# Performance work log

Measured on AMD Instinct MI355X. Metric: run time of the kernel, lower is better.

The kernel has to match this reference:

```python
import jax, jax.numpy as jnp
import numpy as np

N_EDGES = 1_600_000
N_NODES = 100_000
N_GRAPH = 8
D_EDGE = 16
D_NODE = 16
D_GLOB = 16
D_IN = D_EDGE + 2 * D_NODE + D_GLOB  # 64, concat width
D_HID = 64
D_OUT = 16


def setup_inputs() -> dict:
    key = jax.random.key(0)
    ks = jax.random.split(key, 12)
    edges = jax.random.normal(ks[0], (N_EDGES, D_EDGE), dtype=jnp.float32)
    nodes = jax.random.normal(ks[1], (N_NODES, D_NODE), dtype=jnp.float32)
    globals_ = jax.random.normal(ks[2], (N_GRAPH, D_GLOB), dtype=jnp.float32)
    senders = jax.random.randint(ks[3], (N_EDGES,), 0, N_NODES, dtype=jnp.int32)
    receivers = jax.random.randint(ks[4], (N_EDGES,), 0, N_NODES, dtype=jnp.int32)
    edge_graph_ids = jnp.sort(jax.random.randint(ks[5], (N_EDGES,), 0, N_GRAPH, dtype=jnp.int32))
    s0 = 1.0 / np.sqrt(D_IN)
    s1 = 1.0 / np.sqrt(D_HID)
    W0 = jax.random.uniform(ks[6], (D_IN, D_HID), jnp.float32, -s0, s0)
    b0 = jax.random.uniform(ks[7], (D_HID,), jnp.float32, -s0, s0)
    W1 = jax.random.uniform(ks[8], (D_HID, D_HID), jnp.float32, -s1, s1)
    b1 = jax.random.uniform(ks[9], (D_HID,), jnp.float32, -s1, s1)
    W2 = jax.random.uniform(ks[10], (D_HID, D_OUT), jnp.float32, -s1, s1)
    b2 = jax.random.uniform(ks[11], (D_OUT,), jnp.float32, -s1, s1)
    return {"edges": edges, "nodes": nodes, "globals_": globals_,
            "W0": W0, "b0": b0, "W1": W1, "b1": b1, "W2": W2, "b2": b2,
            "senders": senders, "receivers": receivers,
            "edge_graph_ids": edge_graph_ids}


def reference(edges, nodes, globals_, W0, b0, W1, b1, W2, b2,
              senders, receivers, edge_graph_ids):
    # broadcast_receiver/sender_nodes_to_edges: gather node feats per edge
    recv = jnp.take(nodes, receivers, axis=0)          # [E, D_NODE]
    send = jnp.take(nodes, senders, axis=0)            # [E, D_NODE]
    # broadcast_globals_to_edges: repeat(globals, n_edge) == gather by graph id
    glob = jnp.take(globals_, edge_graph_ids, axis=0)  # [E, D_GLOB]
    x = jnp.concatenate([edges, recv, send, glob], axis=-1)  # [E, 64]
    # edge MLP: two hidden relu blocks then output linear (norm='none')
    h = jax.nn.relu(x @ W0 + b0)
    h = jax.nn.relu(h @ W1 + b1)
    return h @ W2 + b2  # updated edges [E, D_OUT]
```

## Files before the change

### kernel.cpp

```cpp
#include <hip/hip_runtime.h>
#include <hip/hip_bf16.h>


typedef float f32x4 __attribute__((ext_vector_type(4)));
typedef short short8 __attribute__((ext_vector_type(8)));

__device__ __forceinline__ unsigned short f2bf(float f) {
    union { float f; unsigned int u; } v; v.f = f;
    unsigned int u = v.u;
    u += 0x7FFFu + ((u >> 16) & 1u);
    return (unsigned short)(u >> 16);
}
__device__ __forceinline__ float bf2f(unsigned short b) {
    union { unsigned int u; float f; } v; v.u = ((unsigned int)b) << 16;
    return v.f;
}
__device__ __forceinline__ void bfsplit(float v, unsigned short& h, unsigned short& l) {
    union { __hip_bfloat16 b; unsigned short u; } ch, cl;
    ch.b = __float2bfloat16(v);
    float r = v - __bfloat162float(ch.b);
    cl.b = __float2bfloat16(r);
    h = ch.u; l = cl.u;
}

__global__ void prep_kernel(const float* __restrict__ W0, const float* __restrict__ b0,
                            const float* __restrict__ W1, const float* __restrict__ b1,
                            const float* __restrict__ W2, const float* __restrict__ b2,
                            void* __restrict__ ws) {
    unsigned short* w0h = (unsigned short*)ws;
    unsigned short* w0l = w0h + 4096;
    unsigned short* w1h = w0h + 8192;
    unsigned short* w1l = w0h + 12288;
    unsigned short* w2h = w0h + 16384;
    unsigned short* w2l = w0h + 17408;
    float* b0f = (float*)(w0h + 18432);
    float* b1f = b0f + 1024;
    float* b2f = b0f + 2048;
    const int tid = blockIdx.x * blockDim.x + threadIdx.x;
    const int gstride = gridDim.x * blockDim.x;

    for (int idx = tid; idx < 4096; idx += gstride) {
        int j = idx & 7, lane = (idx >> 3) & 63, f = idx >> 9;
        int t = f >> 1, kt = f & 1, mr = lane & 15, g = lane >> 4;
        float w = W0[(32 * kt + 8 * g + j) * 64 + (16 * t + mr)];
        unsigned short h = f2bf(w);
        w0h[idx] = h;
        w0l[idx] = f2bf(w - bf2f(h));
    }
    for (int idx = tid; idx < 4096; idx += gstride) {
        int j = idx & 7, lane = (idx >> 3) & 63, f = idx >> 9;
        int t = f >> 1, kt = f & 1, mr = lane & 15, g = lane >> 4;
        int mu = 16 * (2 * kt + (j >> 2)) + 4 * g + (j & 3);
        float w = W1[mu * 64 + (16 * t + mr)];
        unsigned short h = f2bf(w);
        w1h[idx] = h;
        w1l[idx] = f2bf(w - bf2f(h));
    }
    for (int idx = tid; idx < 1024; idx += gstride) {
        int j = idx & 7, lane = (idx >> 3) & 63, kt = idx >> 9;
        int mr = lane & 15, g = lane >> 4;
        int mu = 16 * (2 * kt + (j >> 2)) + 4 * g + (j & 3);
        float w = W2[mu * 16 + mr];
        unsigned short h = f2bf(w);
        w2h[idx] = h;
        w2l[idx] = f2bf(w - bf2f(h));
    }
    for (int idx = tid; idx < 1024; idx += gstride) {
        int lane = idx >> 4, tr = idx & 15;
        int g = lane >> 4, t = tr >> 2, r = tr & 3;
        b0f[idx] = b0[16 * t + 4 * g + r];
        b1f[idx] = b1[16 * t + 4 * g + r];
    }
    for (int idx = tid; idx < 256; idx += gstride) {
        int lane = idx >> 2, r = idx & 3, g = lane >> 4;
        b2f[idx] = b2[4 * g + r];
    }
}

__global__ __launch_bounds__(256, 2) void edge_mlp_kernel(
    const float* __restrict__ edges, const float* __restrict__ nodes,
    const float* __restrict__ globals_, const int* __restrict__ senders,
    const int* __restrict__ receivers, const int* __restrict__ gids,
    const void* __restrict__ ws, float* __restrict__ out, int n_tiles, int iters) {

    const unsigned short* w0h = (const unsigned short*)ws;
    const unsigned short* w0l = w0h + 4096;
    const unsigned short* w1h = w0h + 8192;
    const unsigned short* w1l = w0h + 12288;
    const unsigned short* w2h = w0h + 16384;
    const unsigned short* w2l = w0h + 17408;
    const float* b0f = (const float*)(w0h + 18432);
    const float* b1f = b0f + 1024;
    const float* b2f = b0f + 2048;

    const int lane = threadIdx.x & 63;
    const int wv = threadIdx.x >> 6;
    const int mr = lane & 15;
    const int g = lane >> 4;

    short8 W0H[4][2], W0L[4][2], W1H[4][2], W1L[4][2], W2H[2], W2L[2];
#pragma unroll
    for (int t = 0; t < 4; ++t)
#pragma unroll
        for (int kt = 0; kt < 2; ++kt) {
            int o = ((t * 2 + kt) * 64 + lane) * 8;
            W0H[t][kt] = *(const short8*)(w0h + o);
            W0L[t][kt] = *(const short8*)(w0l + o);
            W1H[t][kt] = *(const short8*)(w1h + o);
            W1L[t][kt] = *(const short8*)(w1l + o);
        }
#pragma unroll
    for (int kt = 0; kt < 2; ++kt) {
        int o = (kt * 64 + lane) * 8;
        W2H[kt] = *(const short8*)(w2h + o);
        W2L[kt] = *(const short8*)(w2l + o);
    }
    float B0[16], B1[16], B2[4];
#pragma unroll
    for (int i = 0; i < 16; ++i) { B0[i] = b0f[lane * 16 + i]; B1[i] = b1f[lane * 16 + i]; }
#pragma unroll
    for (int i = 0; i < 4; ++i) B2[i] = b2f[lane * 4 + i];

    const int W = gridDim.x << 2;
    const int wave_id = (blockIdx.x << 2) | wv;
    const int last = n_tiles - 1;

    #define TILE_OF(i) (((wave_id + (i) * W) < n_tiles) ? (wave_id + (i) * W) : last)

    int e_cur = TILE_OF(0) * 16 + mr;
    {
        int ri = receivers[e_cur], si = senders[e_cur], gi = gids[e_cur];
        (void)ri; (void)si; (void)gi;
    }
    int ri0 = receivers[e_cur], si0 = senders[e_cur], gi0 = gids[e_cur];
    const float* p0 = (g < 2) ? (edges + (size_t)e_cur * 16 + 8 * g)
                              : (nodes + (size_t)ri0 * 16 + 8 * (g - 2));
    const float* p1 = (g < 2) ? (nodes + (size_t)si0 * 16 + 8 * g)
                              : (globals_ + (size_t)gi0 * 16 + 8 * (g - 2));
    f32x4 x0 = *(const f32x4*)p0;
    f32x4 x1 = *(const f32x4*)(p0 + 4);
    f32x4 x2 = *(const f32x4*)p1;
    f32x4 x3 = *(const f32x4*)(p1 + 4);

    int e_nxt = TILE_OF(1) * 16 + mr;
    int ri_n = receivers[e_nxt], si_n = senders[e_nxt], gi_n = gids[e_nxt];

    for (int i = 0; i < iters; ++i) {
        const float* q0 = (g < 2) ? (edges + (size_t)e_nxt * 16 + 8 * g)
                                  : (nodes + (size_t)ri_n * 16 + 8 * (g - 2));
        const float* q1 = (g < 2) ? (nodes + (size_t)si_n * 16 + 8 * g)
                                  : (globals_ + (size_t)gi_n * 16 + 8 * (g - 2));
        f32x4 n0 = *(const f32x4*)q0;
        f32x4 n1 = *(const f32x4*)(q0 + 4);
        f32x4 n2 = *(const f32x4*)q1;
        f32x4 n3 = *(const f32x4*)(q1 + 4);

        int e_nn = TILE_OF(i + 2) * 16 + mr;
        int ri_nn = receivers[e_nn], si_nn = senders[e_nn], gi_nn = gids[e_nn];

        float xs[16];
#pragma unroll
        for (int k = 0; k < 4; ++k) { xs[k] = x0[k]; xs[4 + k] = x1[k]; xs[8 + k] = x2[k]; xs[12 + k] = x3[k]; }
        short8 XH[2], XL[2];
#pragma unroll
        for (int kt = 0; kt < 2; ++kt)
#pragma unroll
            for (int j = 0; j < 8; ++j) {
                unsigned short h, l;
                bfsplit(xs[kt * 8 + j], h, l);
                XH[kt][j] = (short)h;
                XL[kt][j] = (short)l;
            }

        short8 HH[2], HL[2];
#pragma unroll
        for (int t = 0; t < 4; ++t) {
            f32x4 a = {B0[t * 4 + 0], B0[t * 4 + 1], B0[t * 4 + 2], B0[t * 4 + 3]};
            a = __builtin_amdgcn_mfma_f32_16x16x32_bf16(W0L[t][0], XH[0], a, 0, 0, 0);
            a = __builtin_amdgcn_mfma_f32_16x16x32_bf16(W0L[t][1], XH[1], a, 0, 0, 0);
            a = __builtin_amdgcn_mfma_f32_16x16x32_bf16(W0H[t][0], XL[0], a, 0, 0, 0);
            a = __builtin_amdgcn_mfma_f32_16x16x32_bf16(W0H[t][1], XL[1], a, 0, 0, 0);
            a = __builtin_amdgcn_mfma_f32_16x16x32_bf16(W0H[t][0], XH[0], a, 0, 0, 0);
            a = __builtin_amdgcn_mfma_f32_16x16x32_bf16(W0H[t][1], XH[1], a, 0, 0, 0);
#pragma unroll
            for (int r = 0; r < 4; ++r) {
                float v = fmaxf(a[r], 0.0f);
                int kt = t >> 1, j = ((t & 1) << 2) | r;
                unsigned short h, l;
                bfsplit(v, h, l);
                HH[kt][j] = (short)h;
                HL[kt][j] = (short)l;
            }
        }

        short8 GH[2], GL[2];
#pragma unroll
        for (int t = 0; t < 4; ++t) {
            f32x4 a = {B1[t * 4 + 0], B1[t * 4 + 1], B1[t * 4 + 2], B1[t * 4 + 3]};
            a = __builtin_amdgcn_mfma_f32_16x16x32_bf16(W1L[t][0], HH[0], a, 0, 0, 0);
            a = __builtin_amdgcn_mfma_f32_16x16x32_bf16(W1L[t][1], HH[1], a, 0, 0, 0);
            a = __builtin_amdgcn_mfma_f32_16x16x32_bf16(W1H[t][0], HL[0], a, 0, 0, 0);
            a = __builtin_amdgcn_mfma_f32_16x16x32_bf16(W1H[t][1], HL[1], a, 0, 0, 0);
            a = __builtin_amdgcn_mfma_f32_16x16x32_bf16(W1H[t][0], HH[0], a, 0, 0, 0);
            a = __builtin_amdgcn_mfma_f32_16x16x32_bf16(W1H[t][1], HH[1], a, 0, 0, 0);
#pragma unroll
            for (int r = 0; r < 4; ++r) {
                float v = fmaxf(a[r], 0.0f);
                int kt = t >> 1, j = ((t & 1) << 2) | r;
                unsigned short h, l;
                bfsplit(v, h, l);
                GH[kt][j] = (short)h;
                GL[kt][j] = (short)l;
            }
        }

        f32x4 o = {B2[0], B2[1], B2[2], B2[3]};
        o = __builtin_amdgcn_mfma_f32_16x16x32_bf16(W2L[0], GH[0], o, 0, 0, 0);
        o = __builtin_amdgcn_mfma_f32_16x16x32_bf16(W2L[1], GH[1], o, 0, 0, 0);
        o = __builtin_amdgcn_mfma_f32_16x16x32_bf16(W2H[0], GL[0], o, 0, 0, 0);
        o = __builtin_amdgcn_mfma_f32_16x16x32_bf16(W2H[1], GL[1], o, 0, 0, 0);
        o = __builtin_amdgcn_mfma_f32_16x16x32_bf16(W2H[0], GH[0], o, 0, 0, 0);
        o = __builtin_amdgcn_mfma_f32_16x16x32_bf16(W2H[1], GH[1], o, 0, 0, 0);

        __builtin_nontemporal_store(o, (f32x4*)(out + (size_t)e_cur * 16 + 4 * g));

        e_cur = e_nxt;
        x0 = n0; x1 = n1; x2 = n2; x3 = n3;
        e_nxt = e_nn; ri_n = ri_nn; si_n = si_nn; gi_n = gi_nn;
    }
    #undef TILE_OF
}

extern "C" void kernel_launch(void* const* d_in, const int* in_sizes, int n_in,
                              void* d_out, int out_size, void* d_ws, size_t ws_size,
                              hipStream_t stream) {
    const float* edges    = (const float*)d_in[0];
    const float* nodes    = (const float*)d_in[1];
    const float* globals_ = (const float*)d_in[2];
    const float* W0 = (const float*)d_in[3];
    const float* b0 = (const float*)d_in[4];
    const float* W1 = (const float*)d_in[5];
    const float* b1 = (const float*)d_in[6];
    const float* W2 = (const float*)d_in[7];
    const float* b2 = (const float*)d_in[8];
    const int* senders   = (const int*)d_in[9];
    const int* receivers = (const int*)d_in[10];
    const int* gids      = (const int*)d_in[11];
    float* out = (float*)d_out;

    const int n_edges = in_sizes[9];
    const int n_tiles = n_edges >> 4;

    prep_kernel<<<72, 256, 0, stream>>>(W0, b0, W1, b1, W2, b2, d_ws);

    int grid = 2500;
    if (grid > (n_tiles + 3) / 4) grid = (n_tiles + 3) / 4;
    const int waves = grid * 4;
    const int iters = (n_tiles + waves - 1) / waves;
    edge_mlp_kernel<<<grid, 256, 0, stream>>>(edges, nodes, globals_, senders, receivers,
                                              gids, d_ws, out, n_tiles, iters);
}
```

Measured before the change: 282.2 us.

## Stage split-bf16 weights in LDS, pack conversions, dual accumulators, raise occupancy

New measurement: 518.1 us. 83.6% more time.

```diff
diff --git a/kernel.cpp b/kernel.cpp
--- a/kernel.cpp
+++ b/kernel.cpp
@@ -4,23 +4,34 @@
 
 typedef float f32x4 __attribute__((ext_vector_type(4)));
 typedef short short8 __attribute__((ext_vector_type(8)));
+typedef unsigned int u32;
+typedef unsigned int u32x4 __attribute__((ext_vector_type(4)));
 
 __device__ __forceinline__ unsigned short f2bf(float f) {
-    union { float f; unsigned int u; } v; v.f = f;
-    unsigned int u = v.u;
+    union { float f; u32 u; } v; v.f = f;
+    u32 u = v.u;
     u += 0x7FFFu + ((u >> 16) & 1u);
     return (unsigned short)(u >> 16);
 }
 __device__ __forceinline__ float bf2f(unsigned short b) {
-    union { unsigned int u; float f; } v; v.u = ((unsigned int)b) << 16;
+    union { u32 u; float f; } v; v.u = ((u32)b) << 16;
     return v.f;
 }
-__device__ __forceinline__ void bfsplit(float v, unsigned short& h, unsigned short& l) {
-    union { __hip_bfloat16 b; unsigned short u; } ch, cl;
-    ch.b = __float2bfloat16(v);
-    float r = v - __bfloat162float(ch.b);
-    cl.b = __float2bfloat16(r);
-    h = ch.u; l = cl.u;
+__device__ __forceinline__ u32 pk2(float a, float b) {
+    union { __hip_bfloat162 v; u32 u; } c;
+    c.v = __float22bfloat162_rn(make_float2(a, b));
+    return c.u;
+}
+__device__ __forceinline__ float lo_f(u32 p) { union { u32 u; float f; } c; c.u = p << 16; return c.f; }
+__device__ __forceinline__ float hi_f(u32 p) { union { u32 u; float f; } c; c.u = p & 0xffff0000u; return c.f; }
+__device__ __forceinline__ void split4(f32x4 v, u32& h0, u32& h1, u32& l0, u32& l1) {
+    h0 = pk2(v[0], v[1]);
+    h1 = pk2(v[2], v[3]);
+    l0 = pk2(v[0] - lo_f(h0), v[1] - hi_f(h0));
+    l1 = pk2(v[2] - lo_f(h1), v[3] - hi_f(h1));
+}
+__device__ __forceinline__ short8 s8(u32 a, u32 b, u32 c, u32 d) {
+    union { u32x4 u; short8 s; } t; t.u = u32x4{a, b, c, d}; return t.s;
 }
 
 __global__ void prep_kernel(const float* __restrict__ W0, const float* __restrict__ b0,
@@ -66,8 +77,8 @@
         w2l[idx] = f2bf(w - bf2f(h));
     }
     for (int idx = tid; idx < 1024; idx += gstride) {
-        int lane = idx >> 4, tr = idx & 15;
-        int g = lane >> 4, t = tr >> 2, r = tr & 3;
+        int t = idx >> 8, lane = (idx >> 2) & 63, r = idx & 3;
+        int g = lane >> 4;
         b0f[idx] = b0[16 * t + 4 * g + r];
         b1f[idx] = b1[16 * t + 4 * g + r];
     }
@@ -77,61 +88,40 @@
     }
 }
 
-__global__ __launch_bounds__(256, 2) void edge_mlp_kernel(
+__global__ __launch_bounds__(256, 3) void edge_mlp_kernel(
     const float* __restrict__ edges, const float* __restrict__ nodes,
     const float* __restrict__ globals_, const int* __restrict__ senders,
     const int* __restrict__ receivers, const int* __restrict__ gids,
     const void* __restrict__ ws, float* __restrict__ out, int n_tiles, int iters) {
 
-    const unsigned short* w0h = (const unsigned short*)ws;
-    const unsigned short* w0l = w0h + 4096;
-    const unsigned short* w1h = w0h + 8192;
-    const unsigned short* w1l = w0h + 12288;
-    const unsigned short* w2h = w0h + 16384;
-    const unsigned short* w2l = w0h + 17408;
-    const float* b0f = (const float*)(w0h + 18432);
-    const float* b1f = b0f + 1024;
-    const float* b2f = b0f + 2048;
+    __shared__ f32x4 smem4[2880];
+    {
+        const f32x4* src = (const f32x4*)ws;
+        for (int i = threadIdx.x; i < 2880; i += 256) smem4[i] = src[i];
+    }
+    __syncthreads();
+
+    const short8* w0h = (const short8*)smem4;
+    const short8* w0l = w0h + 512;
+    const short8* w1h = w0h + 1024;
+    const short8* w1l = w0h + 1536;
+    const short8* w2h = w0h + 2048;
+    const short8* w2l = w0h + 2176;
+    const f32x4* b0v = smem4 + 2304;
+    const f32x4* b1v = b0v + 256;
+    const f32x4* b2v = b1v + 256;
 
     const int lane = threadIdx.x & 63;
     const int wv = threadIdx.x >> 6;
     const int mr = lane & 15;
     const int g = lane >> 4;
 
-    short8 W0H[4][2], W0L[4][2], W1H[4][2], W1L[4][2], W2H[2], W2L[2];
-#pragma unroll
-    for (int t = 0; t < 4; ++t)
-#pragma unroll
-        for (int kt = 0; kt < 2; ++kt) {
-            int o = ((t * 2 + kt) * 64 + lane) * 8;
-            W0H[t][kt] = *(const short8*)(w0h + o);
-            W0L[t][kt] = *(const short8*)(w0l + o);
-            W1H[t][kt] = *(const short8*)(w1h + o);
-            W1L[t][kt] = *(const short8*)(w1l + o);
-        }
-#pragma unroll
-    for (int kt = 0; kt < 2; ++kt) {
-        int o = (kt * 64 + lane) * 8;
-        W2H[kt] = *(const short8*)(w2h + o);
-        W2L[kt] = *(const short8*)(w2l + o);
-    }
-    float B0[16], B1[16], B2[4];
-#pragma unroll
-    for (int i = 0; i < 16; ++i) { B0[i] = b0f[lane * 16 + i]; B1[i] = b1f[lane * 16 + i]; }
-#pragma unroll
-    for (int i = 0; i < 4; ++i) B2[i] = b2f[lane * 4 + i];
-
     const int W = gridDim.x << 2;
     const int wave_id = (blockIdx.x << 2) | wv;
     const int last = n_tiles - 1;
-
     #define TILE_OF(i) (((wave_id + (i) * W) < n_tiles) ? (wave_id + (i) * W) : last)
 
     int e_cur = TILE_OF(0) * 16 + mr;
-    {
-        int ri = receivers[e_cur], si = senders[e_cur], gi = gids[e_cur];
-        (void)ri; (void)si; (void)gi;
-    }
     int ri0 = receivers[e_cur], si0 = senders[e_cur], gi0 = gids[e_cur];
     const float* p0 = (g < 2) ? (edges + (size_t)e_cur * 16 + 8 * g)
                               : (nodes + (size_t)ri0 * 16 + 8 * (g - 2));
@@ -158,69 +148,86 @@
         int e_nn = TILE_OF(i + 2) * 16 + mr;
         int ri_nn = receivers[e_nn], si_nn = senders[e_nn], gi_nn = gids[e_nn];
 
-        float xs[16];
-#pragma unroll
-        for (int k = 0; k < 4; ++k) { xs[k] = x0[k]; xs[4 + k] = x1[k]; xs[8 + k] = x2[k]; xs[12 + k] = x3[k]; }
-        short8 XH[2], XL[2];
-#pragma unroll
-        for (int kt = 0; kt < 2; ++kt)
-#pragma unroll
-            for (int j = 0; j < 8; ++j) {
-                unsigned short h, l;
-                bfsplit(xs[kt * 8 + j], h, l);
-                XH[kt][j] = (short)h;
-                XL[kt][j] = (short)l;
-            }
-
-        short8 HH[2], HL[2];
+        u32 ah0, ah1, al0, al1, bh0, bh1, bl0, bl1;
+        u32 ch0, ch1, cl0, cl1, dh0, dh1, dl0, dl1;
+        split4(x0, ah0, ah1, al0, al1);
+        split4(x1, bh0, bh1, bl0, bl1);
+        split4(x2, ch0, ch1, cl0, cl1);
+        split4(x3, dh0, dh1, dl0, dl1);
+        short8 XH0 = s8(ah0, ah1, bh0, bh1), XL0 = s8(al0, al1, bl0, bl1);
+        short8 XH1 = s8(ch0, ch1, dh0, dh1), XL1 = s8(cl0, cl1, dl0, dl1);
+
+        u32 HHw[2][4], HLw[2][4];
 #pragma unroll
         for (int t = 0; t < 4; ++t) {
-            f32x4 a = {B0[t * 4 + 0], B0[t * 4 + 1], B0[t * 4 + 2], B0[t * 4 + 3]};
-            a = __builtin_amdgcn_mfma_f32_16x16x32_bf16(W0L[t][0], XH[0], a, 0, 0, 0);
-            a = __builtin_amdgcn_mfma_f32_16x16x32_bf16(W0L[t][1], XH[1], a, 0, 0, 0);
-            a = __builtin_amdgcn_mfma_f32_16x16x32_bf16(W0H[t][0], XL[0], a, 0, 0, 0);
-            a = __builtin_amdgcn_mfma_f32_16x16x32_bf16(W0H[t][1], XL[1], a, 0, 0, 0);
-            a = __builtin_amdgcn_mfma_f32_16x16x32_bf16(W0H[t][0], XH[0], a, 0, 0, 0);
-            a = __builtin_amdgcn_mfma_f32_16x16x32_bf16(W0H[t][1], XH[1], a, 0, 0, 0);
-#pragma unroll
-            for (int r = 0; r < 4; ++r) {
-                float v = fmaxf(a[r], 0.0f);
-                int kt = t >> 1, j = ((t & 1) << 2) | r;
-                unsigned short h, l;
-                bfsplit(v, h, l);
-                HH[kt][j] = (short)h;
-                HL[kt][j] = (short)l;
-            }
+            short8 Wh0 = w0h[(t * 2 + 0) * 64 + lane];
+            short8 Wh1 = w0h[(t * 2 + 1) * 64 + lane];
+            short8 Wl0 = w0l[(t * 2 + 0) * 64 + lane];
+            short8 Wl1 = w0l[(t * 2 + 1) * 64 + lane];
+            f32x4 p = b0v[t * 64 + lane];
+            f32x4 q = {0.f, 0.f, 0.f, 0.f};
+            p = __builtin_amdgcn_mfma_f32_16x16x32_bf16(Wl0, XH0, p, 0, 0, 0);
+            q = __builtin_amdgcn_mfma_f32_16x16x32_bf16(Wl1, XH1, q, 0, 0, 0);
+            p = __builtin_amdgcn_mfma_f32_16x16x32_bf16(Wh0, XL0, p, 0, 0, 0);
+            q = __builtin_amdgcn_mfma_f32_16x16x32_bf16(Wh1, XL1, q, 0, 0, 0);
+            p = __builtin_amdgcn_mfma_f32_16x16x32_bf16(Wh0, XH0, p, 0, 0, 0);
+            q = __builtin_amdgcn_mfma_f32_16x16x32_bf16(Wh1, XH1, q, 0, 0, 0);
+            f32x4 s = p + q;
+            float v0 = fmaxf(s[0], 0.f), v1 = fmaxf(s[1], 0.f);
+            float v2 = fmaxf(s[2], 0.f), v3 = fmaxf(s[3], 0.f);
+            u32 h0 = pk2(v0, v1), h1 = pk2(v2, v3);
+            u32 l0 = pk2(v0 - lo_f(h0), v1 - hi_f(h0));
+            u32 l1 = pk2(v2 - lo_f(h1), v3 - hi_f(h1));
+            int kt = t >> 1, sl = (t & 1) << 1;
+            HHw[kt][sl] = h0; HHw[kt][sl + 1] = h1;
+            HLw[kt][sl] = l0; HLw[kt][sl + 1] = l1;
         }
-
-        short8 GH[2], GL[2];
+        short8 HH0 = s8(HHw[0][0], HHw[0][1], HHw[0][2], HHw[0][3]);
+        short8 HH1 = s8(HHw[1][0], HHw[1][1], HHw[1][2], HHw[1][3]);
+        short8 HL0 = s8(HLw[0][0], HLw[0][1], HLw[0][2], HLw[0][3]);
+        short8 HL1 = s8(HLw[1][0], HLw[1][1], HLw[1][2], HLw[1][3]);
+
+        u32 GHw[2][4], GLw[2][4];
 #pragma unroll
         for (int t = 0; t < 4; ++t) {
-            f32x4 a = {B1[t * 4 + 0], B1[t * 4 + 1], B1[t * 4 + 2], B1[t * 4 + 3]};
-            a = __builtin_amdgcn_mfma_f32_16x16x32_bf16(W1L[t][0], HH[0], a, 0, 0, 0);
-            a = __builtin_amdgcn_mfma_f32_16x16x32_bf16(W1L[t][1], HH[1], a, 0, 0, 0);
-            a = __builtin_amdgcn_mfma_f32_16x16x32_bf16(W1H[t][0], HL[0], a, 0, 0, 0);
-            a = __builtin_amdgcn_mfma_f32_16x16x32_bf16(W1H[t][1], HL[1], a, 0, 0, 0);
-            a = __builtin_amdgcn_mfma_f32_16x16x32_bf16(W1H[t][0], HH[0], a, 0, 0, 0);
-            a = __builtin_amdgcn_mfma_f32_16x16x32_bf16(W1H[t][1], HH[1], a, 0, 0, 0);
-#pragma unroll
-            for (int r = 0; r < 4; ++r) {
-                float v = fmaxf(a[r], 0.0f);
-                int kt = t >> 1, j = ((t & 1) << 2) | r;
-                unsigned short h, l;
-                bfsplit(v, h, l);
-                GH[kt][j] = (short)h;
-                GL[kt][j] = (short)l;
-            }
+            short8 Wh0 = w1h[(t * 2 + 0) * 64 + lane];
+            short8 Wh1 = w1h[(t * 2 + 1) * 64 + lane];
+            short8 Wl0 = w1l[(t * 2 + 0) * 64 + lane];
+            short8 Wl1 = w1l[(t * 2 + 1) * 64 + lane];
+            f32x4 p = b1v[t * 64 + lane];
+            f32x4 q = {0.f, 0.f, 0.f, 0.f};
+            p = __builtin_amdgcn_mfma_f32_16x16x32_bf16(Wl0, HH0, p, 0, 0, 0);
+            q = __builtin_amdgcn_mfma_f32_16x16x32_bf16(Wl1, HH1, q, 0, 0, 0);
+            p = __builtin_amdgcn_mfma_f32_16x16x32_bf16(Wh0, HL0, p, 0, 0, 0);
+            q = __builtin_amdgcn_mfma_f32_16x16x32_bf16(Wh1, HL1, q, 0, 0, 0);
+            p = __builtin_amdgcn_mfma_f32_16x16x32_bf16(Wh0, HH0, p, 0, 0, 0);
+            q = __builtin_amdgcn_mfma_f32_16x16x32_bf16(Wh1, HH1, q, 0, 0, 0);
+            f32x4 s = p + q;
+            float v0 = fmaxf(s[0], 0.f), v1 = fmaxf(s[1], 0.f);
+            float v2 = fmaxf(s[2], 0.f), v3 = fmaxf(s[3], 0.f);
+            u32 h0 = pk2(v0, v1), h1 = pk2(v2, v3);
+            u32 l0 = pk2(v0 - lo_f(h0), v1 - hi_f(h0));
+            u32 l1 = pk2(v2 - lo_f(h1), v3 - hi_f(h1));
+            int kt = t >> 1, sl = (t & 1) << 1;
+            GHw[kt][sl] = h0; GHw[kt][sl + 1] = h1;
+            GLw[kt][sl] = l0; GLw[kt][sl + 1] = l1;
         }
-
-        f32x4 o = {B2[0], B2[1], B2[2], B2[3]};
-        o = __builtin_amdgcn_mfma_f32_16x16x32_bf16(W2L[0], GH[0], o, 0, 0, 0);
-        o = __builtin_amdgcn_mfma_f32_16x16x32_bf16(W2L[1], GH[1], o, 0, 0, 0);
-        o = __builtin_amdgcn_mfma_f32_16x16x32_bf16(W2H[0], GL[0], o, 0, 0, 0);
-        o = __builtin_amdgcn_mfma_f32_16x16x32_bf16(W2H[1], GL[1], o, 0, 0, 0);
-        o = __builtin_amdgcn_mfma_f32_16x16x32_bf16(W2H[0], GH[0], o, 0, 0, 0);
-        o = __builtin_amdgcn_mfma_f32_16x16x32_bf16(W2H[1], GH[1], o, 0, 0, 0);
+        short8 GH0 = s8(GHw[0][0], GHw[0][1], GHw[0][2], GHw[0][3]);
+        short8 GH1 = s8(GHw[1][0], GHw[1][1], GHw[1][2], GHw[1][3]);
+        short8 GL0 = s8(GLw[0][0], GLw[0][1], GLw[0][2], GLw[0][3]);
+        short8 GL1 = s8(GLw[1][0], GLw[1][1], GLw[1][2], GLw[1][3]);
+
+        short8 Vh0 = w2h[lane], Vh1 = w2h[64 + lane];
+        short8 Vl0 = w2l[lane], Vl1 = w2l[64 + lane];
+        f32x4 p = b2v[lane];
+        f32x4 q = {0.f, 0.f, 0.f, 0.f};
+        p = __builtin_amdgcn_mfma_f32_16x16x32_bf16(Vl0, GH0, p, 0, 0, 0);
+        q = __builtin_amdgcn_mfma_f32_16x16x32_bf16(Vl1, GH1, q, 0, 0, 0);
+        p = __builtin_amdgcn_mfma_f32_16x16x32_bf16(Vh0, GL0, p, 0, 0, 0);
+        q = __builtin_amdgcn_mfma_f32_16x16x32_bf16(Vh1, GL1, q, 0, 0, 0);
+        p = __builtin_amdgcn_mfma_f32_16x16x32_bf16(Vh0, GH0, p, 0, 0, 0);
+        q = __builtin_amdgcn_mfma_f32_16x16x32_bf16(Vh1, GH1, q, 0, 0, 0);
+        f32x4 o = p + q;
 
         __builtin_nontemporal_store(o, (f32x4*)(out + (size_t)e_cur * 16 + 4 * g));
 
@@ -253,7 +260,7 @@
 
     prep_kernel<<<72, 256, 0, stream>>>(W0, b0, W1, b1, W2, b2, d_ws);
 
-    int grid = 2500;
+    int grid = 768;
     if (grid > (n_tiles + 3) / 4) grid = (n_tiles + 3) / 4;
     const int waves = grid * 4;
     const int iters = (n_tiles + waves - 1) / waves;
```
